# Kernel tuning notes

Measured on AMD Instinct MI355X. Metric: run time of the kernel, lower is better.

## Reference

```python
import jax, jax.numpy as jnp
import numpy as np

N, HID, MAXD, B, NCLS, GRUH = 50000, 128, 16, 50, 10, 32


def setup_inputs() -> dict:
    key = jax.random.key(0)
    ks = jax.random.split(key, 18)
    s = 0.05
    nrm = lambda k, shp: (jax.random.normal(k, shp, jnp.float32) * s)
    return {
        "feature": jax.random.normal(ks[0], (N, HID), jnp.float32),
        "nbr_idx": jax.random.randint(ks[1], (N, MAXD), 0, N, dtype=jnp.int32),
        "deg": jax.random.randint(ks[2], (N,), 1, MAXD + 1, dtype=jnp.int32),
        "graph_ids": (jnp.arange(N, dtype=jnp.int32) * B) // N,
        # SAGEConv(lstm) params: LSTM(in=HID, hidden=HID) + fc_self/fc_neigh
        "lstm_Wih": nrm(ks[3], (4 * HID, HID)),
        "lstm_Whh": nrm(ks[4], (4 * HID, HID)),
        "lstm_bih": nrm(ks[5], (4 * HID,)),
        "lstm_bhh": nrm(ks[6], (4 * HID,)),
        "W_self": nrm(ks[7], (HID, HID)),
        "W_neigh": nrm(ks[8], (HID, HID)),
        "b_sage": nrm(ks[9], (HID,)),
        # GraphConv params
        "W_gc": nrm(ks[10], (HID, HID)),
        "b_gc": nrm(ks[11], (HID,)),
        # GRU params (h0=0 so weight_hh contributes nothing; only its bias matters)
        "Wih_gru": nrm(ks[12], (3 * GRUH, HID)),
        "bih_gru": nrm(ks[13], (3 * GRUH,)),
        "bhh_gru": nrm(ks[14], (3 * GRUH,)),
        # classifier (dropout is identity at eval)
        "W_cls": nrm(ks[15], (GRUH, NCLS)),
        "b_cls": nrm(ks[16], (NCLS,)),
    }


def _lstm_aggregate(feats, nbr_idx, deg, Wih, Whh, bih, bhh):
    # DGL SAGEConv 'lstm' reducer: run LSTM over each node's neighbor features,
    # take final hidden state. Implemented as a masked scan over padded lists.
    n, hdim = feats.shape
    h0 = jnp.zeros((n, hdim), feats.dtype)

    def step(carry, t):
        h, c = carry
        x = feats[jnp.take(nbr_idx, t, axis=1)]  # [N, HID] gather of t-th neighbor
        gates = x @ Wih.T + bih + h @ Whh.T + bhh
        i, f, g, o = jnp.split(gates, 4, axis=-1)  # torch gate order i,f,g,o
        c_new = jax.nn.sigmoid(f) * c + jax.nn.sigmoid(i) * jnp.tanh(g)
        h_new = jax.nn.sigmoid(o) * jnp.tanh(c_new)
        valid = (t < deg)[:, None]
        return (jnp.where(valid, h_new, h), jnp.where(valid, c_new, c)), None

    (hT, _), _ = jax.lax.scan(step, (h0, h0), jnp.arange(nbr_idx.shape[1]))
    return hT  # hidden at each node's last valid neighbor


def _graph_conv(h, nbr_idx, deg, W, b):
    # DGL GraphConv norm='both': D^-1/2 A D^-1/2 h W + b
    n, maxd = nbr_idx.shape
    norm = jax.lax.rsqrt(jnp.maximum(deg.astype(h.dtype), 1.0))
    hn = h * norm[:, None]
    mask = (jnp.arange(maxd, dtype=jnp.int32)[None, :] < deg[:, None]).astype(h.dtype)
    contrib = hn[nbr_idx.reshape(-1)] * mask.reshape(-1)[:, None]  # [N*MAXD, HID]
    dst = jnp.repeat(jnp.arange(n, dtype=jnp.int32), maxd)
    agg = jax.ops.segment_sum(contrib, dst, num_segments=n)
    return (agg * norm[:, None]) @ W + b


def _gru_step(x, Wih, bih, bhh):
    # single GRU step with h0 = 0 (seq_len == 1 in the original view(1, N, H))
    gh = x @ Wih.T + bih  # [N, 3*GRUH]
    xr, xz, xn = jnp.split(gh, 3, axis=-1)  # torch gate order r,z,n
    br, bz, bn = jnp.split(bhh, 3)
    r = jax.nn.sigmoid(xr + br)
    z = jax.nn.sigmoid(xz + bz)
    nst = jnp.tanh(xn + r * bn)
    return (1.0 - z) * nst  # h' = (1-z)*n + z*h0, h0 = 0


def reference(feature, nbr_idx, deg, graph_ids, lstm_Wih, lstm_Whh, lstm_bih,
              lstm_bhh, W_self, W_neigh, b_sage, W_gc, b_gc, Wih_gru, bih_gru,
              bhh_gru, W_cls, b_cls):
    # conv4: SAGEConv lstm -> relu
    h_nei = _lstm_aggregate(feature, nbr_idx, deg, lstm_Wih, lstm_Whh, lstm_bih, lstm_bhh)
    h = jax.nn.relu(feature @ W_self + h_nei @ W_neigh + b_sage)
    # conv2: GraphConv -> relu
    h = jax.nn.relu(_graph_conv(h, nbr_idx, deg, W_gc, b_gc))
    # GRU over seq_len=1, batch=N
    out = _gru_step(h, Wih_gru, bih_gru, bhh_gru)  # [N, 32]
    # dgl.mean_nodes: per-graph mean pool
    sums = jax.ops.segment_sum(out, graph_ids, num_segments=B)
    cnts = jax.ops.segment_sum(jnp.ones((out.shape[0],), out.dtype), graph_ids, num_segments=B)
    hg = sums / cnts[:, None]
    # classify (Dropout is identity in eval)
    return hg @ W_cls + b_cls  # [B, NCLS]
```

## Files before the change

### kernel.cpp

```cpp
#include <hip/hip_runtime.h>
#include <hip/hip_bf16.h>


#define NN     50000
#define HIDD   128
#define MAXD   16
#define NGRAPH 50
#define NCLSS  10
#define GRUH   32

typedef __attribute__((ext_vector_type(8))) short s16x8;
typedef __attribute__((ext_vector_type(4))) float f32x4;
typedef __hip_bfloat16 bf16;

#define MFMA16(a,b,c)  __builtin_amdgcn_mfma_f32_16x16x32_bf16((a),(b),(c),0,0,0)

__device__ __forceinline__ float bf2f(bf16 x) { return __bfloat162float(x); }
__device__ __forceinline__ bf16  f2bf(float x) { return __float2bfloat16(x); }
__device__ __forceinline__ s16x8 ldfrag(const bf16* p) { return *(const s16x8*)p; }

__device__ __forceinline__ s16x8 ldfrag_f32(const float* p) {
  const float4 a = *(const float4*)p;
  const float4 b = *(const float4*)(p + 4);
  union { s16x8 v; bf16 h[8]; } r;
  r.h[0] = f2bf(a.x); r.h[1] = f2bf(a.y); r.h[2] = f2bf(a.z); r.h[3] = f2bf(a.w);
  r.h[4] = f2bf(b.x); r.h[5] = f2bf(b.y); r.h[6] = f2bf(b.z); r.h[7] = f2bf(b.w);
  return r.v;
}

__device__ __forceinline__ float sigf(float x) {
  return __builtin_amdgcn_rcpf(1.0f + __expf(-x));
}
__device__ __forceinline__ float tanhf_(float x) {
  return 1.0f - 2.0f * __builtin_amdgcn_rcpf(1.0f + __expf(2.0f * x));
}

__device__ __forceinline__ unsigned packbf2(float a, float b) {
  union { bf16 h; unsigned short u; } x, y;
  x.h = f2bf(a); y.h = f2bf(b);
  return (unsigned)x.u | ((unsigned)y.u << 16);
}
__device__ __forceinline__ float lo2f(unsigned u) { return __uint_as_float(u << 16); }
__device__ __forceinline__ float hi2f(unsigned u) { return __uint_as_float(u & 0xffff0000u); }

__device__ __forceinline__ void lgkm_barrier() {
  asm volatile("s_waitcnt lgkmcnt(0)\n\ts_barrier" ::: "memory");
}

__global__ void prep_kernel(const float* __restrict__ feat, const float* __restrict__ Wih,
                            const float* __restrict__ Whh, const float* __restrict__ bih,
                            const float* __restrict__ bhh, const float* __restrict__ Wself,
                            const float* __restrict__ Wneigh, const float* __restrict__ Wgc,
                            const float* __restrict__ Wgru,
                            bf16* featB, bf16* WihB, bf16* WhhB, bf16* WsT, bf16* WnT,
                            bf16* WgT, bf16* WgruB, float* biasS) {
  const int nf = NN * HIDD;
  const int total = nf + 2 * 65536 + 3 * 16384 + 12288 + 512;
  int stride = gridDim.x * blockDim.x;
  for (int idx = blockIdx.x * blockDim.x + threadIdx.x; idx < total; idx += stride) {
    if (idx < nf) { featB[idx] = f2bf(feat[idx]); continue; }
    int j = idx - nf;
    if (j < 65536) { WihB[j] = f2bf(Wih[j]); continue; }
    j -= 65536;
    if (j < 65536) { WhhB[j] = f2bf(Whh[j]); continue; }
    j -= 65536;
    if (j < 16384) { int c = j >> 7, k = j & 127; WsT[j] = f2bf(Wself[k * HIDD + c]); continue; }
    j -= 16384;
    if (j < 16384) { int c = j >> 7, k = j & 127; WnT[j] = f2bf(Wneigh[k * HIDD + c]); continue; }
    j -= 16384;
    if (j < 16384) { int c = j >> 7, k = j & 127; WgT[j] = f2bf(Wgc[k * HIDD + c]); continue; }
    j -= 16384;
    if (j < 12288) { WgruB[j] = f2bf(Wgru[j]); continue; }
    j -= 12288;
    biasS[j] = bih[j] + bhh[j];
  }
}

__global__ __launch_bounds__(256) void hist_kernel(const int* __restrict__ deg, int* hist) {
  __shared__ int lh[17];
  const int tid = threadIdx.x;
  if (tid < 17) lh[tid] = 0;
  __syncthreads();
  const int i = blockIdx.x * 256 + tid;
  if (i < NN) atomicAdd(&lh[deg[i]], 1);
  __syncthreads();
  if (tid < 17 && lh[tid]) atomicAdd(&hist[tid], lh[tid]);
}

__global__ __launch_bounds__(256) void scatter_kernel(const int* __restrict__ deg,
                                                      const int* __restrict__ hist,
                                                      int* __restrict__ resv,
                                                      int* __restrict__ perm) {
  __shared__ int lh[17], lbase[17], lpos[17];
  const int tid = threadIdx.x;
  if (tid < 17) { lh[tid] = 0; lpos[tid] = 0; }
  __syncthreads();
  const int i = blockIdx.x * 256 + tid;
  const int d = (i < NN) ? deg[i] : -1;
  if (d >= 0) atomicAdd(&lh[d], 1);
  __syncthreads();
  if (tid < 17) {
    int pre = 0;
    for (int k = tid + 1; k < 17; ++k) pre += hist[k];
    lbase[tid] = pre + (lh[tid] ? atomicAdd(&resv[tid], lh[tid]) : 0);
  }
  __syncthreads();
  if (d >= 0) {
    const int p = lbase[d] + atomicAdd(&lpos[d], 1);
    perm[p] = i;
  }
}

__global__ __launch_bounds__(256) void ggemm_kernel(const bf16* __restrict__ featB,
                                                    const bf16* __restrict__ WihB,
                                                    const float* __restrict__ biasS,
                                                    bf16* __restrict__ Gp) {
  const int lane = threadIdx.x & 63, wave = threadIdx.x >> 6;
  const int l15 = lane & 15, quad = lane >> 4;
  const int nb = blockIdx.x * 64;

  s16x8 Bx[4][4];
#pragma unroll
  for (int nt = 0; nt < 4; ++nt) {
    int arow = nb + nt * 16 + l15; if (arow >= NN) arow = NN - 1;
#pragma unroll
    for (int kt = 0; kt < 4; ++kt)
      Bx[nt][kt] = ldfrag(featB + (size_t)arow * HIDD + kt * 32 + quad * 8);
  }

  for (int hg = wave * 8; hg < wave * 8 + 8; ++hg) {
    const int wr = (l15 & 3) * HIDD + hg * 4 + (l15 >> 2);
    s16x8 Aw[4];
#pragma unroll
    for (int kt = 0; kt < 4; ++kt)
      Aw[kt] = ldfrag(WihB + (size_t)wr * HIDD + kt * 32 + quad * 8);
    const int hcol = hg * 4 + quad;
    float b0 = biasS[0 * HIDD + hcol], b1 = biasS[1 * HIDD + hcol];
    float b2 = biasS[2 * HIDD + hcol], b3 = biasS[3 * HIDD + hcol];
#pragma unroll
    for (int nt = 0; nt < 4; ++nt) {
      f32x4 acc = {0.f, 0.f, 0.f, 0.f};
#pragma unroll
      for (int kt = 0; kt < 4; ++kt)
        acc = MFMA16(Aw[kt], Bx[nt][kt], acc);
      const int node = nb + nt * 16 + l15;
      if (node < NN) {
        unsigned u0 = packbf2(acc[0] + b0, acc[1] + b1);
        unsigned u1 = packbf2(acc[2] + b2, acc[3] + b3);
        *(uint2*)(Gp + (size_t)node * 512 + hcol * 4) = make_uint2(u0, u1);
      }
    }
  }
}

__global__ __launch_bounds__(1024, 4) void lstm_kernel(const bf16* __restrict__ Gp,
                                                       const bf16* __restrict__ WhhB,
                                                       const int* __restrict__ nbr_idx,
                                                       const int* __restrict__ deg,
                                                       const int* __restrict__ perm,
                                                       bf16* __restrict__ hTB) {
  __shared__ __align__(16) bf16 Hs[2][64 * 128];
  __shared__ int nbr_s[16 * 64];
  __shared__ int nodes_s[64];
  __shared__ int degs_s[64];

  const int tid = threadIdx.x;
  const int lane = tid & 63, w = tid >> 6;
  const int l15 = lane & 15, quad = lane >> 4;
  const int base = blockIdx.x * 64;

  if (tid < 64) {
    const int gi = base + tid;
    const int nd = (gi < NN) ? perm[gi] : -1;
    nodes_s[tid] = nd;
    degs_s[tid] = (nd >= 0) ? deg[nd] : 0;
  }
  __syncthreads();
  {
    const int row = tid & 63, t = tid >> 6;
    const int nd = nodes_s[row];
    nbr_s[t * 64 + row] = (nd >= 0) ? nbr_idx[nd * MAXD + t] : 0;
  }

  s16x8 Bh[2][4];
#pragma unroll
  for (int gt = 0; gt < 2; ++gt) {
    const int wr = (l15 & 3) * HIDD + w * 8 + gt * 4 + (l15 >> 2);
#pragma unroll
    for (int kt = 0; kt < 4; ++kt) {
      Bh[gt][kt] = ldfrag(WhhB + (size_t)wr * HIDD + kt * 32 + quad * 8);
      asm volatile("" : "+v"(Bh[gt][kt]));
    }
  }

  __syncthreads();
  const int maxdeg = degs_s[0];

  int mydeg[4];
#pragma unroll
  for (int nt = 0; nt < 4; ++nt) mydeg[nt] = degs_s[nt * 16 + l15];

  const int gofs0 = (w * 8 + 0 * 4 + quad) * 4;
  const int gofs1 = (w * 8 + 1 * 4 + quad) * 4;

  float cst[2][4] = {{0.f, 0.f, 0.f, 0.f}, {0.f, 0.f, 0.f, 0.f}};
  float hprev[2][4] = {{0.f, 0.f, 0.f, 0.f}, {0.f, 0.f, 0.f, 0.f}};

  for (int t = 0; t < maxdeg; ++t) {
    const int cur = t & 1, nxt = cur ^ 1;

    uint2 gx[2][4];
#pragma unroll
    for (int nt = 0; nt < 4; ++nt) {
      const int nb1 = nbr_s[t * 64 + nt * 16 + l15];
      const bf16* gr = Gp + (size_t)nb1 * 512;
      gx[0][nt] = *(const uint2*)(gr + gofs0);
      gx[1][nt] = *(const uint2*)(gr + gofs1);
    }

    f32x4 acc[2][4];
#pragma unroll
    for (int gt = 0; gt < 2; ++gt)
#pragma unroll
      for (int nt = 0; nt < 4; ++nt) acc[gt][nt] = (f32x4){0.f, 0.f, 0.f, 0.f};

    if (t > 0) {
#pragma unroll
      for (int kt = 0; kt < 4; ++kt) {
#pragma unroll
        for (int nt = 0; nt < 4; ++nt) {
          const int row = nt * 16 + l15;
          const s16x8 ah = ldfrag(Hs[cur] + row * 128 + (((kt * 4 + quad) ^ l15) * 8));
#pragma unroll
          for (int gt = 0; gt < 2; ++gt)
            acc[gt][nt] = MFMA16(Bh[gt][kt], ah, acc[gt][nt]);
        }
      }
    }

#pragma unroll
    for (int gt = 0; gt < 2; ++gt) {
      const int col = w * 8 + gt * 4 + quad;
#pragma unroll
      for (int nt = 0; nt < 4; ++nt) {
        const int row = nt * 16 + l15;
        const uint2 g = gx[gt][nt];
        const float g_i = acc[gt][nt][0] + lo2f(g.x);
        const float g_f = acc[gt][nt][1] + hi2f(g.x);
        const float g_g = acc[gt][nt][2] + lo2f(g.y);
        const float g_o = acc[gt][nt][3] + hi2f(g.y);
        const float iv = sigf(g_i), fv = sigf(g_f);
        const float gv = tanhf_(g_g), ov = sigf(g_o);
        const float cn = fv * cst[gt][nt] + iv * gv;
        const float hn_new = ov * tanhf_(cn);
        const bool act = (t < mydeg[nt]);
        if (act) cst[gt][nt] = cn;
        const float hn = act ? hn_new : hprev[gt][nt];
        hprev[gt][nt] = hn;
        Hs[nxt][row * 128 + ((w ^ (row & 15)) * 8) + (col & 7)] = f2bf(hn);
      }
    }
    lgkm_barrier();
  }

  const bf16* Hf = Hs[maxdeg & 1];
  {
    const int row = tid >> 4, j = tid & 15;
    const int nd = nodes_s[row];
    if (nd >= 0) {
      const s16x8 v = ldfrag(Hf + row * 128 + ((j ^ (row & 15)) * 8));
      *(s16x8*)(hTB + (size_t)nd * HIDD + j * 8) = v;
    }
  }
}

__global__ __launch_bounds__(256) void sage_kernel(const float* __restrict__ featF,
                                                   const bf16* __restrict__ hTB,
                                                   const bf16* __restrict__ WsT,
                                                   const bf16* __restrict__ WnT,
                                                   const float* __restrict__ b_sage,
                                                   const int* __restrict__ deg,
                                                   bf16* __restrict__ h1n) {
  const int lane = threadIdx.x & 63, wave = threadIdx.x >> 6;
  const int l15 = lane & 15, quad = lane >> 4;
  const int nb = blockIdx.x * 64 + wave * 16;
  int arow = nb + l15; if (arow >= NN) arow = NN - 1;
  s16x8 Fa[4], Ha[4];
#pragma unroll
  for (int kt = 0; kt < 4; ++kt) {
    Fa[kt] = ldfrag_f32(featF + (size_t)arow * HIDD + kt * 32 + quad * 8);
    Ha[kt] = ldfrag(hTB + (size_t)arow * HIDD + kt * 32 + quad * 8);
  }
  int nodes[4]; float nrm[4];
#pragma unroll
  for (int r = 0; r < 4; ++r) {
    const int nd = nb + quad * 4 + r;
    nodes[r] = nd;
    nrm[r] = rsqrtf((float)deg[(nd < NN) ? nd : (NN - 1)]);
  }
  for (int ct = 0; ct < 8; ++ct) {
    const int col = ct * 16 + l15;
    f32x4 acc = {0.f, 0.f, 0.f, 0.f};
#pragma unroll
    for (int kt = 0; kt < 4; ++kt) {
      acc = MFMA16(Fa[kt], ldfrag(WsT + col * HIDD + kt * 32 + quad * 8), acc);
      acc = MFMA16(Ha[kt], ldfrag(WnT + col * HIDD + kt * 32 + quad * 8), acc);
    }
    const float bb = b_sage[col];
#pragma unroll
    for (int r = 0; r < 4; ++r)
      if (nodes[r] < NN) {
        const float v = fmaxf(acc[r] + bb, 0.f) * nrm[r];
        h1n[(size_t)nodes[r] * HIDD + col] = f2bf(v);
      }
  }
}

__global__ __launch_bounds__(256) void agg_kernel(const bf16* __restrict__ h1n,
                                                  const int* __restrict__ nbr_idx,
                                                  const int* __restrict__ deg,
                                                  bf16* __restrict__ aggB) {
  const int wave = threadIdx.x >> 6, lane = threadIdx.x & 63;
  const int node = blockIdx.x * 4 + wave;
  if (node >= NN) return;
  const int d = deg[node];
  const int idx_l = nbr_idx[node * MAXD + (lane & 15)];
  const int c = lane * 2;
  float a0 = 0.f, a1 = 0.f;
  for (int t = 0; t < d; ++t) {
    const int nbr = __shfl(idx_l, t, 64);
    const __hip_bfloat162 v = *(const __hip_bfloat162*)(h1n + (size_t)nbr * HIDD + c);
    a0 += __bfloat162float(v.x);
    a1 += __bfloat162float(v.y);
  }
  const float nm = rsqrtf((float)d);
  aggB[(size_t)node * HIDD + c]     = f2bf(a0 * nm);
  aggB[(size_t)node * HIDD + c + 1] = f2bf(a1 * nm);
}

__global__ __launch_bounds__(256) void gcgru_kernel(const bf16* __restrict__ aggB,
                                                    const bf16* __restrict__ WgT,
                                                    const float* __restrict__ b_gc,
                                                    const bf16* __restrict__ WgruB,
                                                    const float* __restrict__ bih,
                                                    const float* __restrict__ bhh,
                                                    float* __restrict__ gout) {
  __shared__ __align__(16) bf16 H2[64 * 136];
  const int lane = threadIdx.x & 63, wave = threadIdx.x >> 6;
  const int l15 = lane & 15, quad = lane >> 4;
  const int nb = blockIdx.x * 64 + wave * 16;
  int arow = nb + l15; if (arow >= NN) arow = NN - 1;
  s16x8 A[4];
#pragma unroll
  for (int kt = 0; kt < 4; ++kt) A[kt] = ldfrag(aggB + (size_t)arow * HIDD + kt * 32 + quad * 8);
  for (int ct = 0; ct < 8; ++ct) {
    const int col = ct * 16 + l15;
    f32x4 acc = {0.f, 0.f, 0.f, 0.f};
#pragma unroll
    for (int kt = 0; kt < 4; ++kt)
      acc = MFMA16(A[kt], ldfrag(WgT + col * HIDD + kt * 32 + quad * 8), acc);
    const float bb = b_gc[col];
#pragma unroll
    for (int r = 0; r < 4; ++r)
      H2[(wave * 16 + quad * 4 + r) * 136 + col] = f2bf(fmaxf(acc[r] + bb, 0.f));
  }
  __syncthreads();
  s16x8 A2[4];
#pragma unroll
  for (int kt = 0; kt < 4; ++kt)
    A2[kt] = ldfrag(H2 + (wave * 16 + l15) * 136 + kt * 32 + quad * 8);
  f32x4 acc[6];
#pragma unroll
  for (int ct = 0; ct < 6; ++ct) {
    f32x4 a = {0.f, 0.f, 0.f, 0.f};
#pragma unroll
    for (int kt = 0; kt < 4; ++kt)
      a = MFMA16(A2[kt], ldfrag(WgruB + (ct * 16 + l15) * HIDD + kt * 32 + quad * 8), a);
    acc[ct] = a;
  }
#pragma unroll
  for (int u = 0; u < 2; ++u) {
    const int cu = 16 * u + l15;
    const float br = bih[cu] + bhh[cu];
    const float bz = bih[32 + cu] + bhh[32 + cu];
    const float bni = bih[64 + cu];
    const float bnh = bhh[64 + cu];
#pragma unroll
    for (int r = 0; r < 4; ++r) {
      const int node = nb + quad * 4 + r;
      if (node < NN) {
        const float rv = sigf(acc[u][r] + br);
        const float zv = sigf(acc[2 + u][r] + bz);
        const float nv = tanhf_(acc[4 + u][r] + bni + rv * bnh);
        gout[(size_t)node * GRUH + cu] = (1.f - zv) * nv;
      }
    }
  }
}

#define POOL_CHUNK 512
__global__ __launch_bounds__(256) void pool_partial_kernel(const float* __restrict__ gout,
                                                           const int* __restrict__ gids,
                                                           float* __restrict__ sums,
                                                           float* __restrict__ cnts) {
  __shared__ float ls[NGRAPH * GRUH];
  __shared__ float lc[NGRAPH];
  const int tid = threadIdx.x;
  for (int i = tid; i < NGRAPH * GRUH; i += 256) ls[i] = 0.f;
  if (tid < NGRAPH) lc[tid] = 0.f;
  __syncthreads();

  const int wave = tid >> 6, lane = tid & 63;
  const int c = lane & 31, half = lane >> 5;
  const int base = blockIdx.x * POOL_CHUNK + wave * (POOL_CHUNK / 8);

  float accv = 0.f, ccnt = 0.f;
  int curg = -1;
  for (int it = 0; it < POOL_CHUNK / 16; ++it) {
    const int n = base + it * 2 + half;
    if (n < NN) {
      const int g = gids[n];
      const float v = gout[(size_t)n * GRUH + c];
      if (g != curg) {
        if (curg >= 0) {
          atomicAdd(&ls[curg * GRUH + c], accv);
          if (c == 0) atomicAdd(&lc[curg], ccnt);
        }
        curg = g; accv = 0.f; ccnt = 0.f;
      }
      accv += v; ccnt += 1.f;
    }
  }
  if (curg >= 0) {
    atomicAdd(&ls[curg * GRUH + c], accv);
    if (c == 0) atomicAdd(&lc[curg], ccnt);
  }
  __syncthreads();
  for (int i = tid; i < NGRAPH * GRUH; i += 256)
    if (ls[i] != 0.f) atomicAdd(&sums[i], ls[i]);
  if (tid < NGRAPH && lc[tid] != 0.f) atomicAdd(&cnts[tid], lc[tid]);
}

__global__ __launch_bounds__(256) void pool_final_kernel(const float* __restrict__ sums,
                                                         const float* __restrict__ cnts,
                                                         const float* __restrict__ Wcls,
                                                         const float* __restrict__ bcls,
                                                         float* __restrict__ out) {
  const int idx = blockIdx.x * blockDim.x + threadIdx.x;
  if (idx >= NGRAPH * NCLSS) return;
  const int g = idx / NCLSS, k = idx % NCLSS;
  const float inv = 1.0f / cnts[g];
  float acc = bcls[k];
#pragma unroll
  for (int cc = 0; cc < GRUH; ++cc)
    acc += sums[g * GRUH + cc] * inv * Wcls[cc * NCLSS + k];
  out[idx] = acc;
}

extern "C" void kernel_launch(void* const* d_in, const int* in_sizes, int n_in,
                              void* d_out, int out_size, void* d_ws, size_t ws_size,
                              hipStream_t stream) {
  const float* feature  = (const float*)d_in[0];
  const int*   nbr_idx  = (const int*)d_in[1];
  const int*   deg      = (const int*)d_in[2];
  const int*   gids     = (const int*)d_in[3];
  const float* lstm_Wih = (const float*)d_in[4];
  const float* lstm_Whh = (const float*)d_in[5];
  const float* lstm_bih = (const float*)d_in[6];
  const float* lstm_bhh = (const float*)d_in[7];
  const float* W_self   = (const float*)d_in[8];
  const float* W_neigh  = (const float*)d_in[9];
  const float* b_sage   = (const float*)d_in[10];
  const float* W_gc     = (const float*)d_in[11];
  const float* b_gc     = (const float*)d_in[12];
  const float* Wih_gru  = (const float*)d_in[13];
  const float* bih_gru  = (const float*)d_in[14];
  const float* bhh_gru  = (const float*)d_in[15];
  const float* W_cls    = (const float*)d_in[16];
  const float* b_cls    = (const float*)d_in[17];

  char* ws = (char*)d_ws;
  bf16*  featB = (bf16*)(ws + 0);
  bf16*  hTB   = (bf16*)(ws + 0);
  float* gout  = (float*)(ws + 0);
  bf16*  Gp    = (bf16*)(ws + 12800000);
  bf16*  h1nB  = (bf16*)(ws + 12800000);
  bf16*  aggB  = (bf16*)(ws + 25600000);
  const size_t wo = 64000000;
  bf16*  WihB  = (bf16*)(ws + wo);
  bf16*  WhhB  = (bf16*)(ws + wo + 131072);
  bf16*  WsT   = (bf16*)(ws + wo + 262144);
  bf16*  WnT   = (bf16*)(ws + wo + 294912);
  bf16*  WgT   = (bf16*)(ws + wo + 327680);
  bf16*  WgruB = (bf16*)(ws + wo + 360448);
  float* biasS = (float*)(ws + wo + 385024);
  int*   perm  = (int*)(ws + 64500000);
  int*   hist  = (int*)(ws + 64800000);
  int*   resv  = hist + 17;
  float* psums = (float*)(ws + 64801216);
  float* pcnts = psums + NGRAPH * GRUH;

  prep_kernel<<<3072, 256, 0, stream>>>(feature, lstm_Wih, lstm_Whh, lstm_bih, lstm_bhh,
                                        W_self, W_neigh, W_gc, Wih_gru,
                                        featB, WihB, WhhB, WsT, WnT, WgT, WgruB, biasS);
  hipMemsetAsync(hist, 0, 34 * sizeof(int), stream);
  hipMemsetAsync(psums, 0, (NGRAPH * GRUH + NGRAPH) * sizeof(float), stream);
  hist_kernel<<<196, 256, 0, stream>>>(deg, hist);
  scatter_kernel<<<196, 256, 0, stream>>>(deg, hist, resv, perm);
  ggemm_kernel<<<782, 256, 0, stream>>>(featB, WihB, biasS, Gp);
  lstm_kernel<<<782, 1024, 0, stream>>>(Gp, WhhB, nbr_idx, deg, perm, hTB);
  sage_kernel<<<782, 256, 0, stream>>>(feature, hTB, WsT, WnT, b_sage, deg, h1nB);
  agg_kernel<<<12500, 256, 0, stream>>>(h1nB, nbr_idx, deg, aggB);
  gcgru_kernel<<<782, 256, 0, stream>>>(aggB, WgT, b_gc, WgruB, bih_gru, bhh_gru, gout);
  pool_partial_kernel<<<(NN + POOL_CHUNK - 1) / POOL_CHUNK, 256, 0, stream>>>(gout, gids, psums, pcnts);
  pool_final_kernel<<<2, 256, 0, stream>>>(psums, pcnts, W_cls, b_cls, (float*)d_out);
}
```

Before: 441.8 us.

## Fuse feature bf16 conversion into gate GEMM and prefetch next-step gate rows in LSTM

After: 516.1 us. 16.8% more time.

```diff
diff --git a/kernel.cpp b/kernel.cpp
--- a/kernel.cpp
+++ b/kernel.cpp
@@ -47,19 +47,17 @@
   asm volatile("s_waitcnt lgkmcnt(0)\n\ts_barrier" ::: "memory");
 }
 
-__global__ void prep_kernel(const float* __restrict__ feat, const float* __restrict__ Wih,
+__global__ __launch_bounds__(256) void prep_kernel(const float* __restrict__ Wih,
                             const float* __restrict__ Whh, const float* __restrict__ bih,
                             const float* __restrict__ bhh, const float* __restrict__ Wself,
                             const float* __restrict__ Wneigh, const float* __restrict__ Wgc,
                             const float* __restrict__ Wgru,
-                            bf16* featB, bf16* WihB, bf16* WhhB, bf16* WsT, bf16* WnT,
+                            bf16* WihB, bf16* WhhB, bf16* WsT, bf16* WnT,
                             bf16* WgT, bf16* WgruB, float* biasS) {
-  const int nf = NN * HIDD;
-  const int total = nf + 2 * 65536 + 3 * 16384 + 12288 + 512;
+  const int total = 2 * 65536 + 3 * 16384 + 12288 + 512;
   int stride = gridDim.x * blockDim.x;
   for (int idx = blockIdx.x * blockDim.x + threadIdx.x; idx < total; idx += stride) {
-    if (idx < nf) { featB[idx] = f2bf(feat[idx]); continue; }
-    int j = idx - nf;
+    int j = idx;
     if (j < 65536) { WihB[j] = f2bf(Wih[j]); continue; }
     j -= 65536;
     if (j < 65536) { WhhB[j] = f2bf(Whh[j]); continue; }
@@ -111,7 +109,7 @@
   }
 }
 
-__global__ __launch_bounds__(256) void ggemm_kernel(const bf16* __restrict__ featB,
+__global__ __launch_bounds__(256) void ggemm_kernel(const float* __restrict__ featF,
                                                     const bf16* __restrict__ WihB,
                                                     const float* __restrict__ biasS,
                                                     bf16* __restrict__ Gp) {
@@ -125,7 +123,7 @@
     int arow = nb + nt * 16 + l15; if (arow >= NN) arow = NN - 1;
 #pragma unroll
     for (int kt = 0; kt < 4; ++kt)
-      Bx[nt][kt] = ldfrag(featB + (size_t)arow * HIDD + kt * 32 + quad * 8);
+      Bx[nt][kt] = ldfrag_f32(featF + (size_t)arow * HIDD + kt * 32 + quad * 8);
   }
 
   for (int hg = wave * 8; hg < wave * 8 + 8; ++hg) {
@@ -206,16 +204,24 @@
   float cst[2][4] = {{0.f, 0.f, 0.f, 0.f}, {0.f, 0.f, 0.f, 0.f}};
   float hprev[2][4] = {{0.f, 0.f, 0.f, 0.f}, {0.f, 0.f, 0.f, 0.f}};
 
-  for (int t = 0; t < maxdeg; ++t) {
-    const int cur = t & 1, nxt = cur ^ 1;
-
-    uint2 gx[2][4];
+  uint2 gxA[2][4], gxB[2][4];
+#pragma unroll
+  for (int nt = 0; nt < 4; ++nt) {
+    const int nb1 = nbr_s[0 * 64 + nt * 16 + l15];
+    const bf16* gr = Gp + (size_t)nb1 * 512;
+    gxA[0][nt] = *(const uint2*)(gr + gofs0);
+    gxA[1][nt] = *(const uint2*)(gr + gofs1);
+  }
+
+  auto step = [&](int T, uint2 (&GXU)[2][4], uint2 (&GXP)[2][4]) {
+    const int cur = T & 1, nxt = cur ^ 1;
+    const int tn = (T + 1 < maxdeg) ? (T + 1) : T;
 #pragma unroll
     for (int nt = 0; nt < 4; ++nt) {
-      const int nb1 = nbr_s[t * 64 + nt * 16 + l15];
+      const int nb1 = nbr_s[tn * 64 + nt * 16 + l15];
       const bf16* gr = Gp + (size_t)nb1 * 512;
-      gx[0][nt] = *(const uint2*)(gr + gofs0);
-      gx[1][nt] = *(const uint2*)(gr + gofs1);
+      GXP[0][nt] = *(const uint2*)(gr + gofs0);
+      GXP[1][nt] = *(const uint2*)(gr + gofs1);
     }
 
     f32x4 acc[2][4];
@@ -224,7 +230,7 @@
 #pragma unroll
       for (int nt = 0; nt < 4; ++nt) acc[gt][nt] = (f32x4){0.f, 0.f, 0.f, 0.f};
 
-    if (t > 0) {
+    if (T > 0) {
 #pragma unroll
       for (int kt = 0; kt < 4; ++kt) {
 #pragma unroll
@@ -244,7 +250,7 @@
 #pragma unroll
       for (int nt = 0; nt < 4; ++nt) {
         const int row = nt * 16 + l15;
-        const uint2 g = gx[gt][nt];
+        const uint2 g = GXU[gt][nt];
         const float g_i = acc[gt][nt][0] + lo2f(g.x);
         const float g_f = acc[gt][nt][1] + hi2f(g.x);
         const float g_g = acc[gt][nt][2] + lo2f(g.y);
@@ -253,7 +259,7 @@
         const float gv = tanhf_(g_g), ov = sigf(g_o);
         const float cn = fv * cst[gt][nt] + iv * gv;
         const float hn_new = ov * tanhf_(cn);
-        const bool act = (t < mydeg[nt]);
+        const bool act = (T < mydeg[nt]);
         if (act) cst[gt][nt] = cn;
         const float hn = act ? hn_new : hprev[gt][nt];
         hprev[gt][nt] = hn;
@@ -261,6 +267,11 @@
       }
     }
     lgkm_barrier();
+  };
+
+  for (int t = 0; t < maxdeg; t += 2) {
+    step(t, gxA, gxB);
+    if (t + 1 < maxdeg) step(t + 1, gxB, gxA);
   }
 
   const bf16* Hf = Hs[maxdeg & 1];
@@ -480,7 +491,6 @@
   const float* b_cls    = (const float*)d_in[17];
 
   char* ws = (char*)d_ws;
-  bf16*  featB = (bf16*)(ws + 0);
   bf16*  hTB   = (bf16*)(ws + 0);
   float* gout  = (float*)(ws + 0);
   bf16*  Gp    = (bf16*)(ws + 12800000);
@@ -500,14 +510,14 @@
   float* psums = (float*)(ws + 64801216);
   float* pcnts = psums + NGRAPH * GRUH;
 
-  prep_kernel<<<3072, 256, 0, stream>>>(feature, lstm_Wih, lstm_Whh, lstm_bih, lstm_bhh,
-                                        W_self, W_neigh, W_gc, Wih_gru,
-                                        featB, WihB, WhhB, WsT, WnT, WgT, WgruB, biasS);
+  prep_kernel<<<754, 256, 0, stream>>>(lstm_Wih, lstm_Whh, lstm_bih, lstm_bhh,
+                                       W_self, W_neigh, W_gc, Wih_gru,
+                                       WihB, WhhB, WsT, WnT, WgT, WgruB, biasS);
   hipMemsetAsync(hist, 0, 34 * sizeof(int), stream);
   hipMemsetAsync(psums, 0, (NGRAPH * GRUH + NGRAPH) * sizeof(float), stream);
   hist_kernel<<<196, 256, 0, stream>>>(deg, hist);
   scatter_kernel<<<196, 256, 0, stream>>>(deg, hist, resv, perm);
-  ggemm_kernel<<<782, 256, 0, stream>>>(featB, WihB, biasS, Gp);
+  ggemm_kernel<<<782, 256, 0, stream>>>(feature, WihB, biasS, Gp);
   lstm_kernel<<<782, 1024, 0, stream>>>(Gp, WhhB, nbr_idx, deg, perm, hTB);
   sage_kernel<<<782, 256, 0, stream>>>(feature, hTB, WsT, WnT, b_sage, deg, h1nB);
   agg_kernel<<<12500, 256, 0, stream>>>(h1nB, nbr_idx, deg, aggB);
```
